# Kernel tuning notes

Measured on AMD Instinct MI355X. Metric: run time of the kernel, lower is better.

Reference implementation:

```python
import jax, jax.numpy as jnp
import numpy as np

V = 100000   # vocab size
E = 300      # embed dim
H = 300      # hidden size
LBL = 5      # label count
LEAVES = 512 # complete binary tree -> N = 2*LEAVES - 1 = 1023 nodes


def _build_tree():
    """Complete binary tree, nodes in topological order (children before parents).
    Returns children_idx [N,2] int32, children_mask [N,2] int32."""
    n = 2 * LEAVES - 1
    children = np.zeros((n, 2), dtype=np.int32)
    mask = np.zeros((n, 2), dtype=np.int32)
    prev_start, prev_size, start = 0, LEAVES, LEAVES
    while prev_size > 1:
        size = prev_size // 2
        for p in range(size):
            node = start + p
            children[node] = [prev_start + 2 * p, prev_start + 2 * p + 1]
            mask[node] = 1
        prev_start, prev_size, start = start, size, start + size
    return jnp.asarray(children), jnp.asarray(mask)


def _linear_params(key, fan_in, fan_out):
    kw, kb = jax.random.split(key)
    bound = 1.0 / np.sqrt(fan_in)
    W = jax.random.uniform(kw, (fan_in, fan_out), minval=-bound, maxval=bound, dtype=jnp.float32)
    b = jax.random.uniform(kb, (fan_out,), minval=-bound, maxval=bound, dtype=jnp.float32)
    return W, b


def setup_inputs() -> dict:
    key = jax.random.key(0)
    ks = jax.random.split(key, 12)
    children_idx, children_mask = _build_tree()
    N = children_idx.shape[0]
    word_ids = jax.random.randint(ks[0], (N,), 0, V, dtype=jnp.int32)
    labels = jax.random.randint(ks[1], (N,), 0, LBL, dtype=jnp.int32)
    emb = jax.random.normal(ks[2], (V, E), dtype=jnp.float32) * 0.1
    W_ix, b_ix = _linear_params(ks[3], E, H)
    W_ih, b_ih = _linear_params(ks[4], H, H)
    W_fx, b_fx = _linear_params(ks[5], E, H)
    W_fh, b_fh = _linear_params(ks[6], H, H)
    W_ux, b_ux = _linear_params(ks[7], E, H)
    W_uh, b_uh = _linear_params(ks[8], H, H)
    W_out, b_out = _linear_params(ks[9], H, LBL)
    return dict(word_ids=word_ids, labels=labels, children_idx=children_idx,
                children_mask=children_mask, emb=emb,
                W_ix=W_ix, b_ix=b_ix, W_ih=W_ih, b_ih=b_ih,
                W_fx=W_fx, b_fx=b_fx, W_fh=W_fh, b_fh=b_fh,
                W_ux=W_ux, b_ux=b_ux, W_uh=W_uh, b_uh=b_uh,
                W_out=W_out, b_out=b_out)


def reference(word_ids, labels, children_idx, children_mask, emb,
              W_ix, b_ix, W_ih, b_ih, W_fx, b_fx, W_fh, b_fh,
              W_ux, b_ux, W_uh, b_uh, W_out, b_out):
    N = word_ids.shape[0]
    x = emb[word_ids]                       # [N,E] embedding lookup
    # Precompute all input projections in one batched GEMM each.
    ix_x = x @ W_ix + b_ix                  # [N,H]
    fx_x = x @ W_fx + b_fx
    ux_x = x @ W_ux + b_ux
    maskf = children_mask.astype(x.dtype)   # [N,2]

    def step(carry, inp):
        c_all, h_all = carry
        t, ch, m, ixx, fxx, uxx = inp       # ch:[2] int, m:[2]
        mc = m[:, None]                     # [2,1]
        ch_h = h_all[ch] * mc               # [2,H] masked gather (leaf -> zeros)
        ch_c = c_all[ch] * mc
        hsum = ch_h.sum(0)                  # child-sum of h
        i = jax.nn.sigmoid(ixx + hsum @ W_ih + b_ih)
        # NOTE: original code (faithfully) uses fx/fh for the o gate and
        # sigmoid (not tanh) for the u gate.
        o = jax.nn.sigmoid(fxx + hsum @ W_fh + b_fh)
        u = jax.nn.sigmoid(uxx + hsum @ W_uh + b_uh)
        f = jax.nn.sigmoid(ch_h @ W_fh + b_fh + fxx)   # [2,H] per-child forget
        c = i * u + (f * ch_c * mc).sum(0)
        h = o * jnp.tanh(c)
        return (c_all.at[t].set(c), h_all.at[t].set(h)), None

    zeros = jnp.zeros((N, H), dtype=x.dtype)
    xs = (jnp.arange(N), children_idx, maskf, ix_x, fx_x, ux_x)
    (c_all, h_all), _ = jax.lax.scan(step, (zeros, zeros), xs)

    logits = h_all @ W_out + b_out          # [N,LBL]
    logp = jax.nn.log_softmax(logits, axis=-1)
    # NLLLoss per node (batch of 1 -> mean == pick), summed over all nodes.
    loss = -logp[jnp.arange(N), labels].sum()
    return logp, loss
```

## Files before the change

kernel.cpp:

```cpp
#include <hip/hip_runtime.h>
#include <math.h>

#define HDIM 300
#define LBL 5

__device__ __forceinline__ float sigmoidf_(float x) {
    return 1.0f / (1.0f + expf(-x));
}

template<int ROWS>
__global__ __launch_bounds__(512)
void proj_kernel(const int* __restrict__ word_ids,
                 const float* __restrict__ emb,
                 const float* __restrict__ W_ix, const float* __restrict__ b_ix,
                 const float* __restrict__ W_fx, const float* __restrict__ b_fx,
                 const float* __restrict__ W_ux, const float* __restrict__ b_ux,
                 float* __restrict__ ixx, float* __restrict__ fxx,
                 float* __restrict__ uxx, int N)
{
    __shared__ float xs[ROWS][HDIM];
    const int t0 = blockIdx.x * ROWS;
    const int tid = threadIdx.x;

    for (int idx = tid; idx < ROWS * HDIM; idx += 512) {
        int r = idx / HDIM;
        int i = idx - r * HDIM;
        int t = t0 + r;
        float v = 0.f;
        if (t < N) {
            size_t w = (size_t)word_ids[t];
            v = emb[w * HDIM + i];
        }
        xs[r][i] = v;
    }
    __syncthreads();

    if (tid >= 450) return;
    const int mat = tid / 150;
    const int jj = (tid - mat * 150) * 2;

    const float* __restrict__ W = (mat == 0) ? W_ix : (mat == 1) ? W_fx : W_ux;
    const float* __restrict__ B = (mat == 0) ? b_ix : (mat == 1) ? b_fx : b_ux;
    float* __restrict__ O       = (mat == 0) ? ixx  : (mat == 1) ? fxx  : uxx;

    float a0[ROWS], a1[ROWS];
#pragma unroll
    for (int r = 0; r < ROWS; r++) { a0[r] = 0.f; a1[r] = 0.f; }

#pragma unroll 6
    for (int i = 0; i < HDIM; i++) {
        float2 w = *(const float2*)(W + (size_t)i * HDIM + jj);
#pragma unroll
        for (int r = 0; r < ROWS; r++) {
            float xv = xs[r][i];
            a0[r] = fmaf(xv, w.x, a0[r]);
            a1[r] = fmaf(xv, w.y, a1[r]);
        }
    }

    const float bb0 = B[jj], bb1 = B[jj + 1];
#pragma unroll
    for (int r = 0; r < ROWS; r++) {
        int t = t0 + r;
        if (t >= N) break;
        O[(size_t)t * HDIM + jj]     = a0[r] + bb0;
        O[(size_t)t * HDIM + jj + 1] = a1[r] + bb1;
    }
}

template<bool FIRST>
__global__ __launch_bounds__(960)
void level_kernel(int level_start,
                  const int* __restrict__ children_idx,
                  const int* __restrict__ children_mask,
                  const float* __restrict__ W_ih, const float* __restrict__ b_ih,
                  const float* __restrict__ W_fh, const float* __restrict__ b_fh,
                  const float* __restrict__ W_uh, const float* __restrict__ b_uh,
                  const float* __restrict__ ixx, const float* __restrict__ fxx,
                  const float* __restrict__ uxx,
                  float* __restrict__ c_all, float* __restrict__ h_all)
{
    __shared__ float h0s[HDIM], h1s[HDIM];
    __shared__ float c0s[HDIM], c1s[HDIM];
    __shared__ float g0s[HDIM], g1s[HDIM], aihs[HDIM], auhs[HDIM];

    const int tid = threadIdx.x;
    const int t   = level_start + blockIdx.x;

    const int c0 = children_idx[2 * t];
    const int c1 = children_idx[2 * t + 1];
    const float m0 = (float)children_mask[2 * t];
    const float m1 = (float)children_mask[2 * t + 1];

    if (FIRST) {
        const int gid = tid / 320;
        const int j   = tid - gid * 320;
        if (gid < 2 && j < HDIM) {
            int ch = (gid == 0) ? c0 : c1;
            float m = (gid == 0) ? m0 : m1;
            size_t o = (size_t)ch * HDIM + j;
            float ig = sigmoidf_(ixx[o] + b_ih[j]);
            float og = sigmoidf_(fxx[o] + b_fh[j]);
            float ug = sigmoidf_(uxx[o] + b_uh[j]);
            float c = ig * ug;
            float h = og * tanhf(c);
            h_all[o] = h;
            if (gid == 0) { h0s[j] = h * m; c0s[j] = c * m; }
            else          { h1s[j] = h * m; c1s[j] = c * m; }
        }
    } else {
        for (int idx = tid; idx < 2 * HDIM; idx += 960) {
            int r = idx < HDIM ? 0 : 1;
            int i = idx - r * HDIM;
            int ch = r ? c1 : c0;
            float m = r ? m1 : m0;
            float hv = h_all[(size_t)ch * HDIM + i] * m;
            if (r) h1s[i] = hv; else h0s[i] = hv;
        }
    }
    __syncthreads();

    const int gid = tid / 320;
    const int j   = tid - gid * 320;
    if (j < HDIM) {
        const float* __restrict__ W = (gid == 0) ? W_ih : (gid == 1) ? W_fh : W_uh;
        float a0 = 0.f, a1 = 0.f;
#pragma unroll 6
        for (int i = 0; i < HDIM; i++) {
            float w = W[(size_t)i * HDIM + j];
            float h0 = h0s[i], h1 = h1s[i];
            if (gid == 1) {
                a0 = fmaf(h0, w, a0);
                a1 = fmaf(h1, w, a1);
            } else {
                a0 = fmaf(h0 + h1, w, a0);
            }
        }
        if (gid == 0)      aihs[j] = a0;
        else if (gid == 1) { g0s[j] = a0; g1s[j] = a1; }
        else               auhs[j] = a0;
    }
    __syncthreads();

    if (tid < HDIM) {
        const int jj = tid;
        size_t o = (size_t)t * HDIM + jj;
        float vix = ixx[o], vfx = fxx[o], vux = uxx[o];
        float g0 = g0s[jj], g1 = g1s[jj];
        float bfh = b_fh[jj];
        float ig = sigmoidf_(vix + aihs[jj] + b_ih[jj]);
        float og = sigmoidf_(vfx + g0 + g1 + bfh);
        float ug = sigmoidf_(vux + auhs[jj] + b_uh[jj]);
        float f0 = sigmoidf_(g0 + bfh + vfx);
        float f1 = sigmoidf_(g1 + bfh + vfx);
        float cc0, cc1;
        if (FIRST) { cc0 = c0s[jj]; cc1 = c1s[jj]; }
        else {
            cc0 = c_all[(size_t)c0 * HDIM + jj] * m0;
            cc1 = c_all[(size_t)c1 * HDIM + jj] * m1;
        }
        float c = ig * ug + f0 * cc0 + f1 * cc1;
        float h = og * tanhf(c);
        c_all[o] = c;
        h_all[o] = h;
    }
}

__global__ __launch_bounds__(64)
void out_kernel(const float* __restrict__ h_all,
                const int* __restrict__ labels,
                const float* __restrict__ W_out, const float* __restrict__ b_out,
                float* __restrict__ out, float* __restrict__ loss, int N)
{
    const int t = blockIdx.x;
    const int l = threadIdx.x;

    float acc[LBL];
#pragma unroll
    for (int k = 0; k < LBL; k++) acc[k] = 0.f;

    for (int i = l; i < HDIM; i += 64) {
        float hv = h_all[(size_t)t * HDIM + i];
#pragma unroll
        for (int k = 0; k < LBL; k++)
            acc[k] = fmaf(hv, W_out[i * LBL + k], acc[k]);
    }

#pragma unroll
    for (int k = 0; k < LBL; k++) {
        float v = acc[k];
        for (int off = 32; off > 0; off >>= 1)
            v += __shfl_down(v, off, 64);
        acc[k] = v;
    }

    if (l == 0) {
        float lg[LBL];
        float mx = -1e30f;
#pragma unroll
        for (int k = 0; k < LBL; k++) {
            lg[k] = acc[k] + b_out[k];
            mx = fmaxf(mx, lg[k]);
        }
        float s = 0.f;
#pragma unroll
        for (int k = 0; k < LBL; k++) s += expf(lg[k] - mx);
        float lse = mx + logf(s);
        int lab = labels[t];
#pragma unroll
        for (int k = 0; k < LBL; k++)
            out[t * LBL + k] = lg[k] - lse;
        atomicAdd(loss, -(lg[lab] - lse));
    }
}

extern "C" void kernel_launch(void* const* d_in, const int* in_sizes, int n_in,
                              void* d_out, int out_size, void* d_ws, size_t ws_size,
                              hipStream_t stream)
{
    const int*   word_ids      = (const int*)d_in[0];
    const int*   labels        = (const int*)d_in[1];
    const int*   children_idx  = (const int*)d_in[2];
    const int*   children_mask = (const int*)d_in[3];
    const float* emb   = (const float*)d_in[4];
    const float* W_ix  = (const float*)d_in[5];  const float* b_ix = (const float*)d_in[6];
    const float* W_ih  = (const float*)d_in[7];  const float* b_ih = (const float*)d_in[8];
    const float* W_fx  = (const float*)d_in[9];  const float* b_fx = (const float*)d_in[10];
    const float* W_fh  = (const float*)d_in[11]; const float* b_fh = (const float*)d_in[12];
    const float* W_ux  = (const float*)d_in[13]; const float* b_ux = (const float*)d_in[14];
    const float* W_uh  = (const float*)d_in[15]; const float* b_uh = (const float*)d_in[16];
    const float* W_out = (const float*)d_in[17]; const float* b_out = (const float*)d_in[18];

    const int N = in_sizes[0];

    float* out  = (float*)d_out;
    float* loss = out + (size_t)N * LBL;

    float* ws    = (float*)d_ws;
    float* ixx   = ws;
    float* fxx   = ixx + (size_t)N * HDIM;
    float* uxx   = fxx + (size_t)N * HDIM;
    float* c_all = uxx + (size_t)N * HDIM;
    float* h_all = c_all + (size_t)N * HDIM;

    hipMemsetAsync(loss, 0, sizeof(float), stream);

    constexpr int ROWS = 4;
    int nb = (N + ROWS - 1) / ROWS;
    proj_kernel<ROWS><<<nb, 512, 0, stream>>>(
        word_ids, emb, W_ix, b_ix, W_fx, b_fx, W_ux, b_ux,
        ixx, fxx, uxx, N);

    const int leaves = (N + 1) / 2;
    int prev = leaves;
    int start = leaves;
    bool first = true;
    while (prev > 1) {
        int size = prev / 2;
        if (first) {
            level_kernel<true><<<size, 960, 0, stream>>>(
                start, children_idx, children_mask,
                W_ih, b_ih, W_fh, b_fh, W_uh, b_uh,
                ixx, fxx, uxx, c_all, h_all);
        } else {
            level_kernel<false><<<size, 960, 0, stream>>>(
                start, children_idx, children_mask,
                W_ih, b_ih, W_fh, b_fh, W_uh, b_uh,
                ixx, fxx, uxx, c_all, h_all);
        }
        first = false;
        prev = size;
        start += size;
    }

    out_kernel<<<N, 64, 0, stream>>>(h_all, labels, W_out, b_out, out, loss, N);
}
```

Baseline: 390.6 us.

## Fuse projection, tree levels and output into one cooperative persistent kernel

```diff
diff --git a/kernel.cpp b/kernel.cpp
--- a/kernel.cpp
+++ b/kernel.cpp
@@ -1,216 +1,232 @@
 #include <hip/hip_runtime.h>
+#include <hip/hip_cooperative_groups.h>
 #include <math.h>
 
+namespace cg = cooperative_groups;
+
 #define HDIM 300
-#define LBL 5
+#define LBL  5
+#define NBLK 256
+#define NTHR 1024
 
 __device__ __forceinline__ float sigmoidf_(float x) {
     return 1.0f / (1.0f + expf(-x));
 }
 
-template<int ROWS>
-__global__ __launch_bounds__(512)
-void proj_kernel(const int* __restrict__ word_ids,
-                 const float* __restrict__ emb,
-                 const float* __restrict__ W_ix, const float* __restrict__ b_ix,
-                 const float* __restrict__ W_fx, const float* __restrict__ b_fx,
-                 const float* __restrict__ W_ux, const float* __restrict__ b_ux,
-                 float* __restrict__ ixx, float* __restrict__ fxx,
-                 float* __restrict__ uxx, int N)
+__global__ __launch_bounds__(NTHR)
+void tree_lstm_kernel(const int* __restrict__ word_ids,
+                      const int* __restrict__ labels,
+                      const int* __restrict__ children_idx,
+                      const int* __restrict__ children_mask,
+                      const float* __restrict__ emb,
+                      const float* __restrict__ W_ix, const float* __restrict__ b_ix,
+                      const float* __restrict__ W_ih, const float* __restrict__ b_ih,
+                      const float* __restrict__ W_fx, const float* __restrict__ b_fx,
+                      const float* __restrict__ W_fh, const float* __restrict__ b_fh,
+                      const float* __restrict__ W_ux, const float* __restrict__ b_ux,
+                      const float* __restrict__ W_uh, const float* __restrict__ b_uh,
+                      const float* __restrict__ W_out, const float* __restrict__ b_out,
+                      float* __restrict__ ixx, float* __restrict__ fxx,
+                      float* __restrict__ uxx,
+                      float* __restrict__ c_all, float* __restrict__ h_all,
+                      float* __restrict__ out, float* __restrict__ loss,
+                      int N)
 {
-    __shared__ float xs[ROWS][HDIM];
-    const int t0 = blockIdx.x * ROWS;
+    cg::grid_group grid = cg::this_grid();
+
+    __shared__ union {
+        struct { float x[4][HDIM]; float li[4][HDIM]; float lf[4][HDIM]; float lu[4][HDIM]; } p;
+        struct { float h0[HDIM]; float h1[HDIM]; float aih[HDIM]; float g0[HDIM]; float g1[HDIM]; float auh[HDIM]; } l;
+        struct { float part[4][4][LBL]; } o;
+    } sm;
+
+    const int b   = blockIdx.x;
     const int tid = threadIdx.x;
-
-    for (int idx = tid; idx < ROWS * HDIM; idx += 512) {
-        int r = idx / HDIM;
-        int i = idx - r * HDIM;
+    const int leaves = (N + 1) / 2;
+    const int t0 = b * 4;
+
+    for (int idx = tid; idx < 4 * HDIM; idx += NTHR) {
+        int r = idx / HDIM, i = idx - r * HDIM;
         int t = t0 + r;
         float v = 0.f;
-        if (t < N) {
-            size_t w = (size_t)word_ids[t];
-            v = emb[w * HDIM + i];
-        }
-        xs[r][i] = v;
+        if (t < N) v = emb[(size_t)word_ids[t] * HDIM + i];
+        sm.p.x[r][i] = v;
     }
     __syncthreads();
 
-    if (tid >= 450) return;
-    const int mat = tid / 150;
-    const int jj = (tid - mat * 150) * 2;
-
-    const float* __restrict__ W = (mat == 0) ? W_ix : (mat == 1) ? W_fx : W_ux;
-    const float* __restrict__ B = (mat == 0) ? b_ix : (mat == 1) ? b_fx : b_ux;
-    float* __restrict__ O       = (mat == 0) ? ixx  : (mat == 1) ? fxx  : uxx;
-
-    float a0[ROWS], a1[ROWS];
-#pragma unroll
-    for (int r = 0; r < ROWS; r++) { a0[r] = 0.f; a1[r] = 0.f; }
-
-#pragma unroll 6
-    for (int i = 0; i < HDIM; i++) {
-        float2 w = *(const float2*)(W + (size_t)i * HDIM + jj);
-#pragma unroll
-        for (int r = 0; r < ROWS; r++) {
-            float xv = xs[r][i];
-            a0[r] = fmaf(xv, w.x, a0[r]);
-            a1[r] = fmaf(xv, w.y, a1[r]);
-        }
-    }
-
-    const float bb0 = B[jj], bb1 = B[jj + 1];
-#pragma unroll
-    for (int r = 0; r < ROWS; r++) {
-        int t = t0 + r;
-        if (t >= N) break;
-        O[(size_t)t * HDIM + jj]     = a0[r] + bb0;
-        O[(size_t)t * HDIM + jj + 1] = a1[r] + bb1;
-    }
-}
-
-template<bool FIRST>
-__global__ __launch_bounds__(960)
-void level_kernel(int level_start,
-                  const int* __restrict__ children_idx,
-                  const int* __restrict__ children_mask,
-                  const float* __restrict__ W_ih, const float* __restrict__ b_ih,
-                  const float* __restrict__ W_fh, const float* __restrict__ b_fh,
-                  const float* __restrict__ W_uh, const float* __restrict__ b_uh,
-                  const float* __restrict__ ixx, const float* __restrict__ fxx,
-                  const float* __restrict__ uxx,
-                  float* __restrict__ c_all, float* __restrict__ h_all)
-{
-    __shared__ float h0s[HDIM], h1s[HDIM];
-    __shared__ float c0s[HDIM], c1s[HDIM];
-    __shared__ float g0s[HDIM], g1s[HDIM], aihs[HDIM], auhs[HDIM];
-
-    const int tid = threadIdx.x;
-    const int t   = level_start + blockIdx.x;
-
-    const int c0 = children_idx[2 * t];
-    const int c1 = children_idx[2 * t + 1];
-    const float m0 = (float)children_mask[2 * t];
-    const float m1 = (float)children_mask[2 * t + 1];
-
-    if (FIRST) {
-        const int gid = tid / 320;
-        const int j   = tid - gid * 320;
-        if (gid < 2 && j < HDIM) {
-            int ch = (gid == 0) ? c0 : c1;
-            float m = (gid == 0) ? m0 : m1;
-            size_t o = (size_t)ch * HDIM + j;
-            float ig = sigmoidf_(ixx[o] + b_ih[j]);
-            float og = sigmoidf_(fxx[o] + b_fh[j]);
-            float ug = sigmoidf_(uxx[o] + b_uh[j]);
-            float c = ig * ug;
-            float h = og * tanhf(c);
-            h_all[o] = h;
-            if (gid == 0) { h0s[j] = h * m; c0s[j] = c * m; }
-            else          { h1s[j] = h * m; c1s[j] = c * m; }
-        }
-    } else {
-        for (int idx = tid; idx < 2 * HDIM; idx += 960) {
-            int r = idx < HDIM ? 0 : 1;
-            int i = idx - r * HDIM;
-            int ch = r ? c1 : c0;
-            float m = r ? m1 : m0;
-            float hv = h_all[(size_t)ch * HDIM + i] * m;
-            if (r) h1s[i] = hv; else h0s[i] = hv;
-        }
-    }
-    __syncthreads();
-
-    const int gid = tid / 320;
-    const int j   = tid - gid * 320;
-    if (j < HDIM) {
-        const float* __restrict__ W = (gid == 0) ? W_ih : (gid == 1) ? W_fh : W_uh;
-        float a0 = 0.f, a1 = 0.f;
+    if (tid < 3 * HDIM) {
+        const int mat = tid / HDIM;
+        const int j   = tid - mat * HDIM;
+        const float* __restrict__ W = (mat == 0) ? W_ix : (mat == 1) ? W_fx : W_ux;
+        const float* __restrict__ B = (mat == 0) ? b_ix : (mat == 1) ? b_fx : b_ux;
+        float* __restrict__ O       = (mat == 0) ? ixx  : (mat == 1) ? fxx  : uxx;
+        float (* __restrict__ L)[HDIM] = (mat == 0) ? sm.p.li : (mat == 1) ? sm.p.lf : sm.p.lu;
+
+        float a0 = 0.f, a1 = 0.f, a2 = 0.f, a3 = 0.f;
 #pragma unroll 6
         for (int i = 0; i < HDIM; i++) {
-            float w = W[(size_t)i * HDIM + j];
-            float h0 = h0s[i], h1 = h1s[i];
-            if (gid == 1) {
-                a0 = fmaf(h0, w, a0);
-                a1 = fmaf(h1, w, a1);
-            } else {
-                a0 = fmaf(h0 + h1, w, a0);
-            }
-        }
-        if (gid == 0)      aihs[j] = a0;
-        else if (gid == 1) { g0s[j] = a0; g1s[j] = a1; }
-        else               auhs[j] = a0;
+            float w = W[i * HDIM + j];
+            a0 = fmaf(sm.p.x[0][i], w, a0);
+            a1 = fmaf(sm.p.x[1][i], w, a1);
+            a2 = fmaf(sm.p.x[2][i], w, a2);
+            a3 = fmaf(sm.p.x[3][i], w, a3);
+        }
+        const float bb = B[j];
+        float v[4] = { a0 + bb, a1 + bb, a2 + bb, a3 + bb };
+#pragma unroll
+        for (int r = 0; r < 4; r++) {
+            int t = t0 + r;
+            if (t < N) O[(size_t)t * HDIM + j] = v[r];
+            L[r][j] = v[r];
+        }
     }
     __syncthreads();
 
     if (tid < HDIM) {
-        const int jj = tid;
-        size_t o = (size_t)t * HDIM + jj;
-        float vix = ixx[o], vfx = fxx[o], vux = uxx[o];
-        float g0 = g0s[jj], g1 = g1s[jj];
-        float bfh = b_fh[jj];
-        float ig = sigmoidf_(vix + aihs[jj] + b_ih[jj]);
-        float og = sigmoidf_(vfx + g0 + g1 + bfh);
-        float ug = sigmoidf_(vux + auhs[jj] + b_uh[jj]);
-        float f0 = sigmoidf_(g0 + bfh + vfx);
-        float f1 = sigmoidf_(g1 + bfh + vfx);
-        float cc0, cc1;
-        if (FIRST) { cc0 = c0s[jj]; cc1 = c1s[jj]; }
-        else {
-            cc0 = c_all[(size_t)c0 * HDIM + jj] * m0;
-            cc1 = c_all[(size_t)c1 * HDIM + jj] * m1;
-        }
-        float c = ig * ug + f0 * cc0 + f1 * cc1;
-        float h = og * tanhf(c);
-        c_all[o] = c;
-        h_all[o] = h;
-    }
-}
-
-__global__ __launch_bounds__(64)
-void out_kernel(const float* __restrict__ h_all,
-                const int* __restrict__ labels,
-                const float* __restrict__ W_out, const float* __restrict__ b_out,
-                float* __restrict__ out, float* __restrict__ loss, int N)
-{
-    const int t = blockIdx.x;
-    const int l = threadIdx.x;
-
-    float acc[LBL];
-#pragma unroll
-    for (int k = 0; k < LBL; k++) acc[k] = 0.f;
-
-    for (int i = l; i < HDIM; i += 64) {
-        float hv = h_all[(size_t)t * HDIM + i];
-#pragma unroll
-        for (int k = 0; k < LBL; k++)
-            acc[k] = fmaf(hv, W_out[i * LBL + k], acc[k]);
-    }
-
-#pragma unroll
-    for (int k = 0; k < LBL; k++) {
-        float v = acc[k];
-        for (int off = 32; off > 0; off >>= 1)
-            v += __shfl_down(v, off, 64);
-        acc[k] = v;
-    }
-
-    if (l == 0) {
-        float lg[LBL];
-        float mx = -1e30f;
+        const int j = tid;
+        const float bih = b_ih[j], bfh = b_fh[j], buh = b_uh[j];
+#pragma unroll
+        for (int r = 0; r < 4; r++) {
+            int t = t0 + r;
+            if (t < leaves && t < N) {
+                float ig = sigmoidf_(sm.p.li[r][j] + bih);
+                float og = sigmoidf_(sm.p.lf[r][j] + bfh);
+                float ug = sigmoidf_(sm.p.lu[r][j] + buh);
+                float c = ig * ug;
+                float h = og * tanhf(c);
+                c_all[(size_t)t * HDIM + j] = c;
+                h_all[(size_t)t * HDIM + j] = h;
+            }
+        }
+    }
+    if (b == 0 && tid == 0) *loss = 0.f;
+
+    grid.sync();
+
+    int prev = leaves, start = leaves;
+    while (prev > 1) {
+        int size = prev / 2;
+        if (b < size) {
+            const int t  = start + b;
+            const int c0 = children_idx[2 * t];
+            const int c1 = children_idx[2 * t + 1];
+            const float m0 = (float)children_mask[2 * t];
+            const float m1 = (float)children_mask[2 * t + 1];
+
+            if (tid < 2 * HDIM) {
+                int r = (tid < HDIM) ? 0 : 1;
+                int i = tid - r * HDIM;
+                int ch = r ? c1 : c0;
+                float m = r ? m1 : m0;
+                float hv = h_all[(size_t)ch * HDIM + i] * m;
+                if (r) sm.l.h1[i] = hv; else sm.l.h0[i] = hv;
+            }
+            __syncthreads();
+
+            if (tid < 3 * HDIM) {
+                const int g = tid / HDIM;
+                const int j = tid - g * HDIM;
+                if (g == 1) {
+                    float a0 = 0.f, a1 = 0.f;
+#pragma unroll 6
+                    for (int i = 0; i < HDIM; i++) {
+                        float w = W_fh[i * HDIM + j];
+                        a0 = fmaf(sm.l.h0[i], w, a0);
+                        a1 = fmaf(sm.l.h1[i], w, a1);
+                    }
+                    sm.l.g0[j] = a0;
+                    sm.l.g1[j] = a1;
+                } else {
+                    const float* __restrict__ W = (g == 0) ? W_ih : W_uh;
+                    float a = 0.f;
+#pragma unroll 6
+                    for (int i = 0; i < HDIM; i++) {
+                        float w = W[i * HDIM + j];
+                        a = fmaf(sm.l.h0[i] + sm.l.h1[i], w, a);
+                    }
+                    if (g == 0) sm.l.aih[j] = a; else sm.l.auh[j] = a;
+                }
+            }
+            __syncthreads();
+
+            if (tid < HDIM) {
+                const int j = tid;
+                size_t o = (size_t)t * HDIM + j;
+                float vix = ixx[o], vfx = fxx[o], vux = uxx[o];
+                float g0 = sm.l.g0[j], g1 = sm.l.g1[j];
+                float bfh = b_fh[j];
+                float ig = sigmoidf_(vix + sm.l.aih[j] + b_ih[j]);
+                float og = sigmoidf_(vfx + g0 + g1 + bfh);
+                float ug = sigmoidf_(vux + sm.l.auh[j] + b_uh[j]);
+                float f0 = sigmoidf_(g0 + bfh + vfx);
+                float f1 = sigmoidf_(g1 + bfh + vfx);
+                float cc0 = c_all[(size_t)c0 * HDIM + j] * m0;
+                float cc1 = c_all[(size_t)c1 * HDIM + j] * m1;
+                float c = ig * ug + f0 * cc0 + f1 * cc1;
+                float h = og * tanhf(c);
+                c_all[o] = c;
+                h_all[o] = h;
+            }
+        }
+        grid.sync();
+        prev = size;
+        start += size;
+    }
+
+    {
+        const int r  = tid >> 8;
+        const int k2 = tid & 255;
+        const int t  = t0 + r;
+
+        float acc[LBL];
+#pragma unroll
+        for (int k = 0; k < LBL; k++) acc[k] = 0.f;
+
+        if (t < N) {
+            for (int i = k2; i < HDIM; i += 256) {
+                float hv = h_all[(size_t)t * HDIM + i];
+#pragma unroll
+                for (int k = 0; k < LBL; k++)
+                    acc[k] = fmaf(hv, W_out[i * LBL + k], acc[k]);
+            }
+        }
 #pragma unroll
         for (int k = 0; k < LBL; k++) {
-            lg[k] = acc[k] + b_out[k];
-            mx = fmaxf(mx, lg[k]);
-        }
-        float s = 0.f;
-#pragma unroll
-        for (int k = 0; k < LBL; k++) s += expf(lg[k] - mx);
-        float lse = mx + logf(s);
-        int lab = labels[t];
-#pragma unroll
-        for (int k = 0; k < LBL; k++)
-            out[t * LBL + k] = lg[k] - lse;
-        atomicAdd(loss, -(lg[lab] - lse));
+            float v = acc[k];
+            for (int off = 32; off > 0; off >>= 1)
+                v += __shfl_down(v, off, 64);
+            acc[k] = v;
+        }
+        const int lane = tid & 63;
+        const int w4   = (tid >> 6) & 3;
+        if (lane == 0) {
+#pragma unroll
+            for (int k = 0; k < LBL; k++) sm.o.part[r][w4][k] = acc[k];
+        }
+        __syncthreads();
+
+        if (tid < 4) {
+            int tt = t0 + tid;
+            if (tt < N) {
+                float lg[LBL];
+                float mx = -1e30f;
+#pragma unroll
+                for (int k = 0; k < LBL; k++) {
+                    lg[k] = sm.o.part[tid][0][k] + sm.o.part[tid][1][k] +
+                            sm.o.part[tid][2][k] + sm.o.part[tid][3][k] + b_out[k];
+                    mx = fmaxf(mx, lg[k]);
+                }
+                float s = 0.f;
+#pragma unroll
+                for (int k = 0; k < LBL; k++) s += expf(lg[k] - mx);
+                float lse = mx + logf(s);
+                int lab = labels[tt];
+#pragma unroll
+                for (int k = 0; k < LBL; k++)
+                    out[tt * LBL + k] = lg[k] - lse;
+                atomicAdd(loss, -(lg[lab] - lse));
+            }
+        }
     }
 }
 
@@ -243,35 +259,17 @@
     float* c_all = uxx + (size_t)N * HDIM;
     float* h_all = c_all + (size_t)N * HDIM;
 
-    hipMemsetAsync(loss, 0, sizeof(float), stream);
-
-    constexpr int ROWS = 4;
-    int nb = (N + ROWS - 1) / ROWS;
-    proj_kernel<ROWS><<<nb, 512, 0, stream>>>(
-        word_ids, emb, W_ix, b_ix, W_fx, b_fx, W_ux, b_ux,
-        ixx, fxx, uxx, N);
-
-    const int leaves = (N + 1) / 2;
-    int prev = leaves;
-    int start = leaves;
-    bool first = true;
-    while (prev > 1) {
-        int size = prev / 2;
-        if (first) {
-            level_kernel<true><<<size, 960, 0, stream>>>(
-                start, children_idx, children_mask,
-                W_ih, b_ih, W_fh, b_fh, W_uh, b_uh,
-                ixx, fxx, uxx, c_all, h_all);
-        } else {
-            level_kernel<false><<<size, 960, 0, stream>>>(
-                start, children_idx, children_mask,
-                W_ih, b_ih, W_fh, b_fh, W_uh, b_uh,
-                ixx, fxx, uxx, c_all, h_all);
-        }
-        first = false;
-        prev = size;
-        start += size;
-    }
-
-    out_kernel<<<N, 64, 0, stream>>>(h_all, labels, W_out, b_out, out, loss, N);
+    int Nv = N;
+    void* args[] = {
+        (void*)&word_ids, (void*)&labels, (void*)&children_idx, (void*)&children_mask,
+        (void*)&emb,
+        (void*)&W_ix, (void*)&b_ix, (void*)&W_ih, (void*)&b_ih,
+        (void*)&W_fx, (void*)&b_fx, (void*)&W_fh, (void*)&b_fh,
+        (void*)&W_ux, (void*)&b_ux, (void*)&W_uh, (void*)&b_uh,
+        (void*)&W_out, (void*)&b_out,
+        (void*)&ixx, (void*)&fxx, (void*)&uxx, (void*)&c_all, (void*)&h_all,
+        (void*)&out, (void*)&loss, (void*)&Nv
+    };
+    hipLaunchCooperativeKernel((const void*)tree_lstm_kernel,
+                               dim3(NBLK), dim3(NTHR), args, 0, stream);
 }
```

Result: slower. 675.4 us (+72.9%).
